# Kernel tuning notes

Hardware: AMD Instinct MI355X
Metric: run time of the kernel (lower is better)

Reference implementation:

```python
import jax, jax.numpy as jnp
from jax import lax
import numpy as np

B, S, D, H = 4, 2048, 1024, 16
HD = D // H
EPS = 1e-8
LN_EPS = 1e-5


def setup_inputs() -> dict:
    key = jax.random.key(0)
    ks = jax.random.split(key, 8)
    sc = 1.0 / np.sqrt(D)  # ~ torch Linear default init scale
    return {
        "x": jax.random.normal(ks[0], (B, S, D), jnp.float32),
        "time_mix_r": jnp.full((1, 1, D), 0.5, jnp.float32),
        "time_mix_k": jnp.full((1, 1, D), 0.5, jnp.float32),
        "time_mix_v": jnp.full((1, 1, D), 0.5, jnp.float32),
        "W_r": jax.random.normal(ks[1], (D, D), jnp.float32) * sc,
        "W_k": jax.random.normal(ks[2], (D, D), jnp.float32) * sc,
        "W_v": jax.random.normal(ks[3], (D, D), jnp.float32) * sc,
        "W_o": jax.random.normal(ks[4], (D, D), jnp.float32) * sc,
        "time_decay": jax.random.normal(ks[5], (H, HD), jnp.float32) * 0.1 - 5.0,
        "time_first": jax.random.normal(ks[6], (H, HD), jnp.float32) * 0.1,
        "ln_gamma": jnp.ones((D,), jnp.float32),
        "ln_beta": jnp.zeros((D,), jnp.float32),
    }


def reference(x, time_mix_r, time_mix_k, time_mix_v, W_r, W_k, W_v, W_o,
              time_decay, time_first, ln_gamma, ln_beta):
    b, s, d = x.shape
    h, hd = time_decay.shape
    # token shift: shifted[t] = x[t-1], zeros at t=0
    shifted = jnp.pad(x[:, :-1, :], ((0, 0), (1, 0), (0, 0)))
    xr = x * time_mix_r + shifted * (1.0 - time_mix_r)
    xk = x * time_mix_k + shifted * (1.0 - time_mix_k)
    xv = x * time_mix_v + shifted * (1.0 - time_mix_v)
    r = (xr @ W_r.T).reshape(b, s, h, hd)
    k = (xk @ W_k.T).reshape(b, s, h, hd)
    v = (xv @ W_v.T).reshape(b, s, h, hd)

    w = -jnp.exp(time_decay)   # (h, hd), negative decay
    u = time_first             # (h, hd)

    def step(carry, kv):
        a, bst = carry          # (b,h,hd) each: numerator state, log-denominator state
        kt, vt = kv             # (b,h,hd)
        wk = kt + u
        p = jnp.maximum(bst, wk)
        e1 = jnp.exp(bst - p)
        e2 = jnp.exp(wk - p)
        out = (e1 * a + e2 * vt) / (e1 + e2 + EPS)
        ww = bst + w
        p2 = jnp.maximum(ww, kt)
        e1b = jnp.exp(ww - p2)
        e2b = jnp.exp(kt - p2)
        a_new = e1b * a + e2b * vt
        b_new = p2 + jnp.log(e1b + e2b + EPS)
        return (a_new, b_new), out

    a0 = jnp.zeros((b, h, hd), x.dtype)
    b0 = jnp.full((b, h, hd), -1e38, x.dtype)
    kT = jnp.moveaxis(k, 1, 0)  # (s,b,h,hd)
    vT = jnp.moveaxis(v, 1, 0)
    _, outs = lax.scan(step, (a0, b0), (kT, vT))
    wkv = jnp.moveaxis(outs, 0, 1)  # (b,s,h,hd)

    rwkv = jax.nn.sigmoid(r) * wkv  # (b,s,h,hd)
    # GroupNorm(num_groups=h, channels=d) applied over (channel-within-group, seq)
    mean = jnp.mean(rwkv, axis=(1, 3), keepdims=True)
    var = jnp.var(rwkv, axis=(1, 3), keepdims=True)
    normed = (rwkv - mean) * lax.rsqrt(var + LN_EPS)
    normed = normed * ln_gamma.reshape(1, 1, h, hd) + ln_beta.reshape(1, 1, h, hd)
    return normed.reshape(b, s, d) @ W_o.T
```

## Files before the change

### kernel.cpp

```cpp
#include <hip/hip_runtime.h>
#include <cstdint>
#include <cstddef>

#define B_  4
#define S_  2048
#define D_  1024
#define H_  16
#define HD_ 64
#define M_  (B_ * S_)

#define CHUNKS_ 64
#define CL_     32

typedef __bf16 bf16_t;
typedef bf16_t bf16x8 __attribute__((ext_vector_type(8)));
typedef float  floatx4 __attribute__((ext_vector_type(4)));

__device__ __forceinline__ void async_copy16(const void* gmem, void* lds) {
  __builtin_amdgcn_global_load_lds(
      (__attribute__((address_space(1))) void*)const_cast<void*>(gmem),
      (__attribute__((address_space(3))) void*)lds,
      16, 0, 0);
}

__global__ void pre_kernel(const float* __restrict__ w0, const float* __restrict__ w1,
                           const float* __restrict__ w2, const float* __restrict__ w3,
                           bf16_t* __restrict__ wout,
                           const float* __restrict__ x,
                           const float* __restrict__ tmr, const float* __restrict__ tmk,
                           const float* __restrict__ tmv,
                           bf16_t* __restrict__ xr, bf16_t* __restrict__ xk,
                           bf16_t* __restrict__ xv) {
  const int ONE_M = 1 << 20;
  int gid = blockIdx.x * blockDim.x + threadIdx.x;
  if (gid < 4 * ONE_M) {
    const float* src = (gid < ONE_M) ? w0 : (gid < 2 * ONE_M) ? w1 : (gid < 3 * ONE_M) ? w2 : w3;
    wout[gid] = (bf16_t)src[gid & (ONE_M - 1)];
  } else {
    int idx = gid - 4 * ONE_M;
    int d = idx & (D_ - 1);
    int t = (idx / D_) & (S_ - 1);
    float xc = x[idx];
    float xp = (t == 0) ? 0.0f : x[idx - D_];
    float mr = tmr[d], mk = tmk[d], mv = tmv[d];
    xr[idx] = (bf16_t)(xc * mr + xp * (1.0f - mr));
    xk[idx] = (bf16_t)(xc * mk + xp * (1.0f - mk));
    xv[idx] = (bf16_t)(xc * mv + xp * (1.0f - mv));
  }
}

#define STG(kt, la, lb, p) do {                                            \
    const char* _ga = Abase + (size_t)(kt) * 128;                          \
    const char* _gb = Bbase + (size_t)(kt) * 128;                          \
    async_copy16(_ga + (size_t)(((p) * 2 + 0) * 64 + r8) * 2048 + cbs,     \
                 (la) + ((p) * 2 + 0) * 8192 + tid * 16);                  \
    async_copy16(_ga + (size_t)(((p) * 2 + 1) * 64 + r8) * 2048 + cbs,     \
                 (la) + ((p) * 2 + 1) * 8192 + tid * 16);                  \
    async_copy16(_gb + (size_t)((p) * 64 + r8) * 2048 + cbs,               \
                 (lb) + (p) * 8192 + tid * 16);                            \
  } while (0)

#define PH1(la, lb, STMT) do {                                             \
    _Pragma("unroll")                                                      \
    for (int _j = 0; _j < 4; ++_j) {                                       \
      const char* _rb = (lb) + (wn * 64 + _j * 16 + l15) * 128;            \
      bfr[_j][0] = *(const bf16x8*)(_rb + ((quad * 16) ^ swz));            \
      bfr[_j][1] = *(const bf16x8*)(_rb + ((64 + quad * 16) ^ swz));       \
    }                                                                      \
    _Pragma("unroll")                                                      \
    for (int _i = 0; _i < 2; ++_i) {                                       \
      const char* _ra = (la) + (wm * 64 + _i * 16 + l15) * 128;            \
      afr[_i][0] = *(const bf16x8*)(_ra + ((quad * 16) ^ swz));            \
      afr[_i][1] = *(const bf16x8*)(_ra + ((64 + quad * 16) ^ swz));       \
    }                                                                      \
    STMT;                                                                  \
    asm volatile("s_waitcnt lgkmcnt(0)" ::: "memory");                     \
    __builtin_amdgcn_sched_barrier(0);                                     \
    __builtin_amdgcn_s_setprio(1);                                         \
    _Pragma("unroll")                                                      \
    for (int _k = 0; _k < 2; ++_k)                                         \
      _Pragma("unroll")                                                    \
      for (int _i = 0; _i < 2; ++_i)                                       \
        _Pragma("unroll")                                                  \
        for (int _j = 0; _j < 4; ++_j)                                     \
          acc[_i][_j] = __builtin_amdgcn_mfma_f32_16x16x32_bf16(           \
              afr[_i][_k], bfr[_j][_k], acc[_i][_j], 0, 0, 0);             \
    __builtin_amdgcn_s_setprio(0);                                         \
  } while (0)

#define PH2(la, STMT) do {                                                 \
    _Pragma("unroll")                                                      \
    for (int _i = 0; _i < 2; ++_i) {                                       \
      const char* _ra = (la) + (wm * 64 + (2 + _i) * 16 + l15) * 128;      \
      afr[_i][0] = *(const bf16x8*)(_ra + ((quad * 16) ^ swz));            \
      afr[_i][1] = *(const bf16x8*)(_ra + ((64 + quad * 16) ^ swz));       \
    }                                                                      \
    STMT;                                                                  \
    asm volatile("s_waitcnt lgkmcnt(0)" ::: "memory");                     \
    __builtin_amdgcn_sched_barrier(0);                                     \
    __builtin_amdgcn_s_setprio(1);                                         \
    _Pragma("unroll")                                                      \
    for (int _k = 0; _k < 2; ++_k)                                         \
      _Pragma("unroll")                                                    \
      for (int _i = 0; _i < 2; ++_i)                                       \
        _Pragma("unroll")                                                  \
        for (int _j = 0; _j < 4; ++_j)                                     \
          acc[2 + _i][_j] = __builtin_amdgcn_mfma_f32_16x16x32_bf16(       \
              afr[_i][_k], bfr[_j][_k], acc[2 + _i][_j], 0, 0, 0);         \
    __builtin_amdgcn_s_setprio(0);                                         \
  } while (0)

#define FENCE_BAR(N) do {                                                  \
    asm volatile("s_waitcnt vmcnt(" #N ")" ::: "memory");                  \
    __builtin_amdgcn_s_barrier();                                          \
    asm volatile("" ::: "memory");                                         \
  } while (0)

template <typename CT>
__device__ __forceinline__ void gemm_core(const bf16_t* __restrict__ A,
                                          const bf16_t* __restrict__ Bw,
                                          CT* __restrict__ C, int m0, int n0) {
  __shared__ __align__(16) bf16_t As[3][256][64];
  __shared__ __align__(16) bf16_t Bs[3][128][64];

  const int tid  = threadIdx.x;
  const int lane = tid & 63;
  const int wave = tid >> 6;
  const int wm   = wave >> 1;
  const int wn   = wave & 1;
  const int l15  = lane & 15;
  const int quad = lane >> 4;
  const int r8   = tid >> 3;
  const int cbs  = (((tid & 7) ^ (r8 & 7)) << 4);
  const int swz  = (l15 & 7) << 4;

  const char* Abase = (const char*)(A + (size_t)m0 * D_);
  const char* Bbase = (const char*)(Bw + (size_t)n0 * D_);

  char* const a0 = (char*)&As[0][0][0];
  char* const a1 = a0 + 32768;
  char* const a2 = a1 + 32768;
  char* const b0 = (char*)&Bs[0][0][0];
  char* const b1 = b0 + 16384;
  char* const b2 = b1 + 16384;

  floatx4 acc[4][4] = {};
  bf16x8 afr[2][2], bfr[4][2];

  STG(0, a0, b0, 0); STG(0, a0, b0, 1);
  STG(1, a1, b1, 0); STG(1, a1, b1, 1);
  FENCE_BAR(6);

  char *aC = a0, *aN = a1, *aF = a2;
  char *bC = b0, *bN = b1, *bF = b2;

#pragma unroll 1
  for (int t = 0; t < 14; ++t) {
    PH1(aC, bC, STG(t + 2, aF, bF, 0));
    PH2(aC,     STG(t + 2, aF, bF, 1));
    FENCE_BAR(6);
    char* x;
    x = aC; aC = aN; aN = aF; aF = x;
    x = bC; bC = bN; bN = bF; bF = x;
  }
  PH1(aC, bC, (void)0);
  PH2(aC,     (void)0);
  FENCE_BAR(0);
  PH1(aN, bN, (void)0);
  PH2(aN,     (void)0);

#pragma unroll
  for (int i = 0; i < 4; ++i) {
#pragma unroll
    for (int j = 0; j < 4; ++j) {
      int row = m0 + wm * 64 + i * 16 + quad * 4;
      int col = n0 + wn * 64 + j * 16 + l15;
      CT* Cp = C + (size_t)row * D_ + col;
#pragma unroll
      for (int r = 0; r < 4; ++r)
        Cp[(size_t)r * D_] = (CT)acc[i][j][r];
    }
  }
}

__global__ __launch_bounds__(512, 2)
void gemm3(const bf16_t* __restrict__ xr, const bf16_t* __restrict__ xk,
           const bf16_t* __restrict__ xv, const bf16_t* __restrict__ Wall,
           bf16_t* __restrict__ rbuf, bf16_t* __restrict__ kbuf, bf16_t* __restrict__ vbuf) {
  const int flat = blockIdx.x;
  const int idx  = (flat & 7) * 96 + (flat >> 3);
  const int proj = idx >> 8;
  const int tt   = idx & 255;
  const int mb   = tt >> 3;
  const int nb   = tt & 7;
  const bf16_t* A  = (proj == 0) ? xr : (proj == 1) ? xk : xv;
  const bf16_t* Bw = Wall + (size_t)proj * (1 << 20);
  bf16_t* C = (proj == 0) ? rbuf : (proj == 1) ? kbuf : vbuf;
  gemm_core<bf16_t>(A, Bw, C, mb * 256, nb * 128);
}

__global__ __launch_bounds__(512, 2)
void gemm_bt(const bf16_t* __restrict__ A, const bf16_t* __restrict__ Bw,
             float* __restrict__ C) {
  const int flat = blockIdx.x;
  const int idx  = (flat & 7) * 32 + (flat >> 3);
  const int mb   = idx >> 3;
  const int nb   = idx & 7;
  gemm_core<float>(A, Bw, C, mb * 256, nb * 128);
}

__device__ __forceinline__ void stage_chunk_bf16(const char* gsrc, char* lds, int lane) {
  const int row = lane >> 3;
  const int cb  = (lane & 7) * 16;
#pragma unroll
  for (int i = 0; i < 4; ++i) {
    size_t go = (size_t)(i * 8 + row) * (D_ * 2) + cb;
    async_copy16(gsrc + go, lds + i * 1024 + lane * 16);
  }
}

__global__ __launch_bounds__(64)
void wkv_pass1(const bf16_t* __restrict__ kbuf, const float* __restrict__ time_decay,
               float* __restrict__ G) {
  __shared__ __align__(16) bf16_t ks[CL_][64];
  const int blk   = blockIdx.x;
  const int chunk = blk & (CHUNKS_ - 1);
  const int bh    = blk >> 6;
  const int b = bh >> 4, h = bh & 15;
  const int lane = threadIdx.x;
  const int c = h * HD_ + lane;
  const float w = -__expf(time_decay[c]);

  const size_t gbase = ((size_t)b * S_ + (size_t)chunk * CL_) * D_ + h * HD_;
  stage_chunk_bf16((const char*)(kbuf + gbase), (char*)&ks[0][0], lane);
  __builtin_amdgcn_s_waitcnt(0);
  __syncthreads();

  float g = -1e38f;
  for (int t = 0; t < CL_; ++t) {
    float kt = (float)ks[t][lane];
    float ww = g + w;
    float d2 = ww - kt;
    float em = __expf(-fabsf(d2));
    float e1b = (d2 >= 0.0f) ? 1.0f : em;
    float e2b = (d2 >= 0.0f) ? em : 1.0f;
    g = fmaxf(ww, kt) + __logf(e1b + e2b + 1e-8f);
  }
  G[(size_t)bh * (CHUNKS_ * 64) + chunk * 64 + lane] = g;
}

__global__ __launch_bounds__(64)
void wkv_pass2(const bf16_t* __restrict__ kbuf, const bf16_t* __restrict__ vbuf,
               const float* __restrict__ time_decay, const float* __restrict__ G,
               float* __restrict__ si_b, float* __restrict__ cs_A, float* __restrict__ cs_Bv) {
  __shared__ __align__(16) float Gs[CHUNKS_][64];
  __shared__ __align__(16) bf16_t ks[CL_][64];
  __shared__ __align__(16) bf16_t vs[CL_][64];
  const int blk   = blockIdx.x;
  const int chunk = blk & (CHUNKS_ - 1);
  const int bh    = blk >> 6;
  const int b = bh >> 4, h = bh & 15;
  const int lane = threadIdx.x;
  const int c = h * HD_ + lane;
  const float w  = -__expf(time_decay[c]);
  const float wL = w * (float)CL_;

  const char* gg = (const char*)(G + (size_t)bh * (CHUNKS_ * 64));
#pragma unroll
  for (int i = 0; i < 16; ++i)
    async_copy16(gg + i * 1024 + lane * 16, (char*)&Gs[0][0] + i * 1024 + lane * 16);

  const size_t gbase = ((size_t)b * S_ + (size_t)chunk * CL_) * D_ + h * HD_;
  stage_chunk_bf16((const char*)(kbuf + gbase), (char*)&ks[0][0], lane);
  stage_chunk_bf16((const char*)(vbuf + gbase), (char*)&vs[0][0], lane);
  __builtin_amdgcn_s_waitcnt(0);
  __syncthreads();

  float bst = -1e38f;
  for (int ch = 0; ch < chunk; ++ch) {
    float g = Gs[ch][lane];
    float b1 = bst + wL;
    float dd = b1 - g;
    float em = __expf(-fabsf(dd));
    bst = fmaxf(b1, g) + __logf(1.0f + em);
  }
  const size_t so = (size_t)bh * (CHUNKS_ * 64) + chunk * 64 + lane;
  si_b[so] = bst;

  float a = 0.0f, Ap = 1.0f;
  for (int t = 0; t < CL_; ++t) {
    float kt = (float)ks[t][lane], vt = (float)vs[t][lane];
    float ww = bst + w;
    float d2 = ww - kt;
    float em = __expf(-fabsf(d2));
    float e1b = (d2 >= 0.0f) ? 1.0f : em;
    float e2b = (d2 >= 0.0f) ? em : 1.0f;
    a  = e1b * a + e2b * vt;
    Ap = Ap * e1b;
    bst = fmaxf(ww, kt) + __logf(e1b + e2b + 1e-8f);
  }
  cs_A [so] = Ap;
  cs_Bv[so] = a;
}

__global__ __launch_bounds__(64)
void wkv_pass3(const bf16_t* __restrict__ rbuf, const bf16_t* __restrict__ kbuf,
               const bf16_t* __restrict__ vbuf,
               const float* __restrict__ time_decay, const float* __restrict__ time_first,
               const float* __restrict__ si_b,
               const float* __restrict__ cs_A, const float* __restrict__ cs_Bv,
               bf16_t* __restrict__ rwkv, float* __restrict__ psum, float* __restrict__ psq) {
  __shared__ __align__(16) char smem[32 * 1024];
  float (*As_)[64] = (float(*)[64])smem;
  float (*Bs_)[64] = (float(*)[64])(smem + 16384);
  const int blk   = blockIdx.x;
  const int chunk = blk & (CHUNKS_ - 1);
  const int bh    = blk >> 6;
  const int b = bh >> 4, h = bh & 15;
  const int lane = threadIdx.x;
  const int c = h * HD_ + lane;
  const float w = -__expf(time_decay[c]);
  const float u = time_first[c];

  const char* ag = (const char*)(cs_A  + (size_t)bh * (CHUNKS_ * 64));
  const char* bg = (const char*)(cs_Bv + (size_t)bh * (CHUNKS_ * 64));
#pragma unroll
  for (int i = 0; i < 16; ++i) {
    async_copy16(ag + i * 1024 + lane * 16, (char*)&As_[0][0] + i * 1024 + lane * 16);
    async_copy16(bg + i * 1024 + lane * 16, (char*)&Bs_[0][0] + i * 1024 + lane * 16);
  }
  const size_t so = (size_t)bh * (CHUNKS_ * 64) + chunk * 64 + lane;
  float bst = si_b[so];
  __builtin_amdgcn_s_waitcnt(0);
  __syncthreads();

  float a = 0.0f;
  for (int ch = 0; ch < chunk; ++ch)
    a = As_[ch][lane] * a + Bs_[ch][lane];
  __syncthreads();

  bf16_t (*rs)[64] = (bf16_t(*)[64])smem;
  bf16_t (*ks)[64] = (bf16_t(*)[64])(smem + 4096);
  bf16_t (*vs)[64] = (bf16_t(*)[64])(smem + 8192);
  const size_t gbase = ((size_t)b * S_ + (size_t)chunk * CL_) * D_ + h * HD_;
  stage_chunk_bf16((const char*)(rbuf + gbase), (char*)&rs[0][0], lane);
  stage_chunk_bf16((const char*)(kbuf + gbase), (char*)&ks[0][0], lane);
  stage_chunk_bf16((const char*)(vbuf + gbase), (char*)&vs[0][0], lane);
  __builtin_amdgcn_s_waitcnt(0);
  __syncthreads();

  float sum = 0.0f, sq = 0.0f;
  size_t widx = gbase + lane;
  for (int t = 0; t < CL_; ++t) {
    float kt = (float)ks[t][lane], vt = (float)vs[t][lane], rt = (float)rs[t][lane];
    float wk = kt + u;
    float d1 = bst - wk;
    float em1 = __expf(-fabsf(d1));
    float e1 = (d1 >= 0.0f) ? 1.0f : em1;
    float e2 = (d1 >= 0.0f) ? em1 : 1.0f;
    float out = __fdividef(e1 * a + e2 * vt, e1 + e2 + 1e-8f);

    float ww = bst + w;
    float d2 = ww - kt;
    float em2 = __expf(-fabsf(d2));
    float e1b = (d2 >= 0.0f) ? 1.0f : em2;
    float e2b = (d2 >= 0.0f) ? em2 : 1.0f;
    a   = e1b * a + e2b * vt;
    bst = fmaxf(ww, kt) + __logf(e1b + e2b + 1e-8f);

    float sig = __fdividef(1.0f, 1.0f + __expf(-rt));
    float o2 = sig * out;
    rwkv[widx] = (bf16_t)o2;
    sum += o2; sq += o2 * o2;
    widx += D_;
  }

#pragma unroll
  for (int off = 32; off > 0; off >>= 1) {
    sum += __shfl_down(sum, off);
    sq  += __shfl_down(sq, off);
  }
  if (lane == 0) {
    psum[bh * CHUNKS_ + chunk] = sum;
    psq [bh * CHUNKS_ + chunk] = sq;
  }
}

__global__ __launch_bounds__(256)
void norm_cast(const bf16_t* __restrict__ rwkv,
               const float* __restrict__ psum, const float* __restrict__ psq,
               const float* __restrict__ gamma, const float* __restrict__ beta,
               bf16_t* __restrict__ normed) {
  __shared__ float smean[4], srstd[4];
  const int tid = threadIdx.x;
  const int lane = tid & 63;
  const int wj = tid >> 6;
  int idx0 = blockIdx.x * 256;
  int d0 = idx0 & (D_ - 1);
  int bb = idx0 / (S_ * D_);
  int bh = bb * H_ + (d0 >> 6) + wj;

  float s = psum[bh * CHUNKS_ + lane];
  float q = psq [bh * CHUNKS_ + lane];
#pragma unroll
  for (int off = 32; off > 0; off >>= 1) {
    s += __shfl_down(s, off);
    q += __shfl_down(q, off);
  }
  if (lane == 0) {
    const float n = (float)(S_ * HD_);
    float mean = s / n;
    float var  = q / n - mean * mean;
    smean[wj] = mean;
    srstd[wj] = rsqrtf(var + 1e-5f);
  }
  __syncthreads();

  int idx = idx0 + tid;
  int d = idx & (D_ - 1);
  float v = ((float)rwkv[idx] - smean[wj]) * srstd[wj] * gamma[d] + beta[d];
  normed[idx] = (bf16_t)v;
}

extern "C" void kernel_launch(void* const* d_in, const int* in_sizes, int n_in,
                              void* d_out, int out_size, void* d_ws, size_t ws_size,
                              hipStream_t stream) {
  const float* x     = (const float*)d_in[0];
  const float* tmr   = (const float*)d_in[1];
  const float* tmk   = (const float*)d_in[2];
  const float* tmv   = (const float*)d_in[3];
  const float* Wr    = (const float*)d_in[4];
  const float* Wk    = (const float*)d_in[5];
  const float* Wv    = (const float*)d_in[6];
  const float* Wo    = (const float*)d_in[7];
  const float* td    = (const float*)d_in[8];
  const float* tf    = (const float*)d_in[9];
  const float* gamma = (const float*)d_in[10];
  const float* beta  = (const float*)d_in[11];

  char* ws = (char*)d_ws;
  const size_t MB = 1024 * 1024;
  bf16_t* W_bf    = (bf16_t*)(ws + 0 * MB);
  bf16_t* Wo_bf   = (bf16_t*)(ws + 6 * MB);
  bf16_t* xr      = (bf16_t*)(ws + 8 * MB);
  bf16_t* xk      = (bf16_t*)(ws + 24 * MB);
  bf16_t* xv      = (bf16_t*)(ws + 40 * MB);
  float*  G       = (float*)(ws + 24 * MB);
  float*  cs_A    = (float*)(ws + 25 * MB);
  float*  cs_Bv   = (float*)(ws + 26 * MB);
  float*  si_b    = (float*)(ws + 27 * MB);
  float*  psum    = (float*)(ws + 28 * MB);
  float*  psq     = (float*)(ws + 28 * MB + 64 * 1024);
  bf16_t* rwkv    = (bf16_t*)(ws + 30 * MB);
  bf16_t* rbuf    = (bf16_t*)(ws + 56 * MB);
  bf16_t* kbuf    = (bf16_t*)(ws + 72 * MB);
  bf16_t* vbuf    = (bf16_t*)(ws + 88 * MB);
  bf16_t* normed  = xr;

  float* outp = (float*)d_out;

  pre_kernel<<<(12 * 1024 * 1024) / 256, 256, 0, stream>>>(
      Wr, Wk, Wv, Wo, W_bf, x, tmr, tmk, tmv, xr, xk, xv);

  gemm3<<<768, 512, 0, stream>>>(xr, xk, xv, W_bf, rbuf, kbuf, vbuf);

  wkv_pass1<<<B_ * H_ * CHUNKS_, 64, 0, stream>>>(kbuf, td, G);
  wkv_pass2<<<B_ * H_ * CHUNKS_, 64, 0, stream>>>(kbuf, vbuf, td, G, si_b, cs_A, cs_Bv);
  wkv_pass3<<<B_ * H_ * CHUNKS_, 64, 0, stream>>>(rbuf, kbuf, vbuf, td, tf,
                                                  si_b, cs_A, cs_Bv, rwkv, psum, psq);

  norm_cast<<<(M_ * D_) / 256, 256, 0, stream>>>(rwkv, psum, psq, gamma, beta, normed);

  gemm_bt<<<256, 512, 0, stream>>>(normed, Wo_bf, outp);
}
```

Baseline: 300.6 us.

## Fuse WKV chunked scan passes and GroupNorm into one per-head kernel; vectorize preprocessing

Replaces the three WKV chunk passes and the separate norm kernel with one kernel per (batch, head). Sixteen wavefronts each handle a 128-step chunk and exchange chunk states and norm partial sums through shared memory, which removes launches and global round-trips for the intermediate state. The preprocessing kernel now converts weights and token-shift mixes four elements per thread with vector loads and stores. The trade-off is only 64 blocks of 1024 threads, so many CUs sit idle. Each thread also runs a longer serial scan, reading k/v/r straight from global memory with strided accesses instead of staging them in LDS.

```diff
diff --git a/kernel.cpp b/kernel.cpp
--- a/kernel.cpp
+++ b/kernel.cpp
@@ -9,11 +9,12 @@
 #define HD_ 64
 #define M_  (B_ * S_)
 
-#define CHUNKS_ 64
-#define CL_     32
+#define WC_ 16
+#define WL_ 128
 
 typedef __bf16 bf16_t;
 typedef bf16_t bf16x8 __attribute__((ext_vector_type(8)));
+typedef bf16_t bf16x4 __attribute__((ext_vector_type(4)));
 typedef float  floatx4 __attribute__((ext_vector_type(4)));
 
 __device__ __forceinline__ void async_copy16(const void* gmem, void* lds) {
@@ -31,21 +32,41 @@
                            const float* __restrict__ tmv,
                            bf16_t* __restrict__ xr, bf16_t* __restrict__ xk,
                            bf16_t* __restrict__ xv) {
-  const int ONE_M = 1 << 20;
+  const int WQ = 1 << 18;
   int gid = blockIdx.x * blockDim.x + threadIdx.x;
-  if (gid < 4 * ONE_M) {
-    const float* src = (gid < ONE_M) ? w0 : (gid < 2 * ONE_M) ? w1 : (gid < 3 * ONE_M) ? w2 : w3;
-    wout[gid] = (bf16_t)src[gid & (ONE_M - 1)];
+  if (gid < 4 * WQ) {
+    int sel = gid >> 18;
+    const float* src = sel == 0 ? w0 : sel == 1 ? w1 : sel == 2 ? w2 : w3;
+    int e = (gid & (WQ - 1)) << 2;
+    const float4 v = *(const float4*)(src + e);
+    bf16x4 o = { (bf16_t)v.x, (bf16_t)v.y, (bf16_t)v.z, (bf16_t)v.w };
+    *(bf16x4*)(wout + ((size_t)gid << 2)) = o;
   } else {
-    int idx = gid - 4 * ONE_M;
-    int d = idx & (D_ - 1);
-    int t = (idx / D_) & (S_ - 1);
-    float xc = x[idx];
-    float xp = (t == 0) ? 0.0f : x[idx - D_];
-    float mr = tmr[d], mk = tmk[d], mv = tmv[d];
-    xr[idx] = (bf16_t)(xc * mr + xp * (1.0f - mr));
-    xk[idx] = (bf16_t)(xc * mk + xp * (1.0f - mk));
-    xv[idx] = (bf16_t)(xc * mv + xp * (1.0f - mv));
+    int g2 = gid - 4 * WQ;
+    size_t idx = (size_t)g2 << 2;
+    int d = (int)(idx & (D_ - 1));
+    int t = (int)((idx >> 10) & (S_ - 1));
+    float4 xc = *(const float4*)(x + idx);
+    float4 xp = make_float4(0.f, 0.f, 0.f, 0.f);
+    if (t != 0) xp = *(const float4*)(x + idx - D_);
+    float4 mr = *(const float4*)(tmr + d);
+    float4 mk = *(const float4*)(tmk + d);
+    float4 mv = *(const float4*)(tmv + d);
+    bf16x4 orv = { (bf16_t)(xc.x * mr.x + xp.x * (1.f - mr.x)),
+                   (bf16_t)(xc.y * mr.y + xp.y * (1.f - mr.y)),
+                   (bf16_t)(xc.z * mr.z + xp.z * (1.f - mr.z)),
+                   (bf16_t)(xc.w * mr.w + xp.w * (1.f - mr.w)) };
+    bf16x4 okv = { (bf16_t)(xc.x * mk.x + xp.x * (1.f - mk.x)),
+                   (bf16_t)(xc.y * mk.y + xp.y * (1.f - mk.y)),
+                   (bf16_t)(xc.z * mk.z + xp.z * (1.f - mk.z)),
+                   (bf16_t)(xc.w * mk.w + xp.w * (1.f - mk.w)) };
+    bf16x4 ovv = { (bf16_t)(xc.x * mv.x + xp.x * (1.f - mv.x)),
+                   (bf16_t)(xc.y * mv.y + xp.y * (1.f - mv.y)),
+                   (bf16_t)(xc.z * mv.z + xp.z * (1.f - mv.z)),
+                   (bf16_t)(xc.w * mv.w + xp.w * (1.f - mv.w)) };
+    *(bf16x4*)(xr + idx) = orv;
+    *(bf16x4*)(xk + idx) = okv;
+    *(bf16x4*)(xv + idx) = ovv;
   }
 }
 
@@ -209,217 +230,143 @@
   gemm_core<float>(A, Bw, C, mb * 256, nb * 128);
 }
 
-__device__ __forceinline__ void stage_chunk_bf16(const char* gsrc, char* lds, int lane) {
-  const int row = lane >> 3;
-  const int cb  = (lane & 7) * 16;
-#pragma unroll
-  for (int i = 0; i < 4; ++i) {
-    size_t go = (size_t)(i * 8 + row) * (D_ * 2) + cb;
-    async_copy16(gsrc + go, lds + i * 1024 + lane * 16);
-  }
-}
-
-__global__ __launch_bounds__(64)
-void wkv_pass1(const bf16_t* __restrict__ kbuf, const float* __restrict__ time_decay,
-               float* __restrict__ G) {
-  __shared__ __align__(16) bf16_t ks[CL_][64];
-  const int blk   = blockIdx.x;
-  const int chunk = blk & (CHUNKS_ - 1);
-  const int bh    = blk >> 6;
+__global__ __launch_bounds__(1024)
+void wkv_gn(const bf16_t* __restrict__ rbuf, const bf16_t* __restrict__ kbuf,
+            const bf16_t* __restrict__ vbuf,
+            const float* __restrict__ time_decay, const float* __restrict__ time_first,
+            const float* __restrict__ gamma, const float* __restrict__ beta,
+            bf16_t* __restrict__ rwkv, bf16_t* __restrict__ normed) {
+  __shared__ float Gs[WC_][64];
+  __shared__ float As_[WC_][64];
+  __shared__ float Bs_[WC_][64];
+  __shared__ float redS[WC_], redQ[WC_];
+  __shared__ float s_stats[2];
+
+  const int bh    = blockIdx.x;
+  const int tid   = threadIdx.x;
+  const int chunk = tid >> 6;
+  const int lane  = tid & 63;
   const int b = bh >> 4, h = bh & 15;
-  const int lane = threadIdx.x;
-  const int c = h * HD_ + lane;
-  const float w = -__expf(time_decay[c]);
-
-  const size_t gbase = ((size_t)b * S_ + (size_t)chunk * CL_) * D_ + h * HD_;
-  stage_chunk_bf16((const char*)(kbuf + gbase), (char*)&ks[0][0], lane);
-  __builtin_amdgcn_s_waitcnt(0);
-  __syncthreads();
-
-  float g = -1e38f;
-  for (int t = 0; t < CL_; ++t) {
-    float kt = (float)ks[t][lane];
-    float ww = g + w;
-    float d2 = ww - kt;
-    float em = __expf(-fabsf(d2));
-    float e1b = (d2 >= 0.0f) ? 1.0f : em;
-    float e2b = (d2 >= 0.0f) ? em : 1.0f;
-    g = fmaxf(ww, kt) + __logf(e1b + e2b + 1e-8f);
-  }
-  G[(size_t)bh * (CHUNKS_ * 64) + chunk * 64 + lane] = g;
-}
-
-__global__ __launch_bounds__(64)
-void wkv_pass2(const bf16_t* __restrict__ kbuf, const bf16_t* __restrict__ vbuf,
-               const float* __restrict__ time_decay, const float* __restrict__ G,
-               float* __restrict__ si_b, float* __restrict__ cs_A, float* __restrict__ cs_Bv) {
-  __shared__ __align__(16) float Gs[CHUNKS_][64];
-  __shared__ __align__(16) bf16_t ks[CL_][64];
-  __shared__ __align__(16) bf16_t vs[CL_][64];
-  const int blk   = blockIdx.x;
-  const int chunk = blk & (CHUNKS_ - 1);
-  const int bh    = blk >> 6;
-  const int b = bh >> 4, h = bh & 15;
-  const int lane = threadIdx.x;
-  const int c = h * HD_ + lane;
-  const float w  = -__expf(time_decay[c]);
-  const float wL = w * (float)CL_;
-
-  const char* gg = (const char*)(G + (size_t)bh * (CHUNKS_ * 64));
-#pragma unroll
-  for (int i = 0; i < 16; ++i)
-    async_copy16(gg + i * 1024 + lane * 16, (char*)&Gs[0][0] + i * 1024 + lane * 16);
-
-  const size_t gbase = ((size_t)b * S_ + (size_t)chunk * CL_) * D_ + h * HD_;
-  stage_chunk_bf16((const char*)(kbuf + gbase), (char*)&ks[0][0], lane);
-  stage_chunk_bf16((const char*)(vbuf + gbase), (char*)&vs[0][0], lane);
-  __builtin_amdgcn_s_waitcnt(0);
-  __syncthreads();
-
-  float bst = -1e38f;
-  for (int ch = 0; ch < chunk; ++ch) {
-    float g = Gs[ch][lane];
-    float b1 = bst + wL;
-    float dd = b1 - g;
-    float em = __expf(-fabsf(dd));
-    bst = fmaxf(b1, g) + __logf(1.0f + em);
-  }
-  const size_t so = (size_t)bh * (CHUNKS_ * 64) + chunk * 64 + lane;
-  si_b[so] = bst;
-
-  float a = 0.0f, Ap = 1.0f;
-  for (int t = 0; t < CL_; ++t) {
-    float kt = (float)ks[t][lane], vt = (float)vs[t][lane];
-    float ww = bst + w;
-    float d2 = ww - kt;
-    float em = __expf(-fabsf(d2));
-    float e1b = (d2 >= 0.0f) ? 1.0f : em;
-    float e2b = (d2 >= 0.0f) ? em : 1.0f;
-    a  = e1b * a + e2b * vt;
-    Ap = Ap * e1b;
-    bst = fmaxf(ww, kt) + __logf(e1b + e2b + 1e-8f);
-  }
-  cs_A [so] = Ap;
-  cs_Bv[so] = a;
-}
-
-__global__ __launch_bounds__(64)
-void wkv_pass3(const bf16_t* __restrict__ rbuf, const bf16_t* __restrict__ kbuf,
-               const bf16_t* __restrict__ vbuf,
-               const float* __restrict__ time_decay, const float* __restrict__ time_first,
-               const float* __restrict__ si_b,
-               const float* __restrict__ cs_A, const float* __restrict__ cs_Bv,
-               bf16_t* __restrict__ rwkv, float* __restrict__ psum, float* __restrict__ psq) {
-  __shared__ __align__(16) char smem[32 * 1024];
-  float (*As_)[64] = (float(*)[64])smem;
-  float (*Bs_)[64] = (float(*)[64])(smem + 16384);
-  const int blk   = blockIdx.x;
-  const int chunk = blk & (CHUNKS_ - 1);
-  const int bh    = blk >> 6;
-  const int b = bh >> 4, h = bh & 15;
-  const int lane = threadIdx.x;
   const int c = h * HD_ + lane;
   const float w = -__expf(time_decay[c]);
   const float u = time_first[c];
 
-  const char* ag = (const char*)(cs_A  + (size_t)bh * (CHUNKS_ * 64));
-  const char* bg = (const char*)(cs_Bv + (size_t)bh * (CHUNKS_ * 64));
+  const size_t gbase = ((size_t)b * S_ + (size_t)chunk * WL_) * D_ + h * HD_ + lane;
+  const bf16_t* kg = kbuf + gbase;
+  const bf16_t* vg = vbuf + gbase;
+  const bf16_t* rg = rbuf + gbase;
+
+  {
+    float g = -1e38f;
+#pragma unroll 4
+    for (int t = 0; t < WL_; ++t) {
+      float kt = (float)kg[(size_t)t * D_];
+      float ww = g + w;
+      float d2 = ww - kt;
+      float em = __expf(-fabsf(d2));
+      float e1b = (d2 >= 0.0f) ? 1.0f : em;
+      float e2b = (d2 >= 0.0f) ? em : 1.0f;
+      g = fmaxf(ww, kt) + __logf(e1b + e2b + 1e-8f);
+    }
+    Gs[chunk][lane] = g;
+  }
+  __syncthreads();
+
+  const float wL = w * (float)WL_;
+  float bst = -1e38f;
+  for (int ch = 0; ch < chunk; ++ch) {
+    float gv = Gs[ch][lane];
+    float b1 = bst + wL;
+    float dd = b1 - gv;
+    float em = __expf(-fabsf(dd));
+    bst = fmaxf(b1, gv) + __logf(1.0f + em);
+  }
+  const float bst_in = bst;
+
+  {
+    float a = 0.0f, Ap = 1.0f;
+#pragma unroll 4
+    for (int t = 0; t < WL_; ++t) {
+      float kt = (float)kg[(size_t)t * D_];
+      float vt = (float)vg[(size_t)t * D_];
+      float ww = bst + w;
+      float d2 = ww - kt;
+      float em = __expf(-fabsf(d2));
+      float e1b = (d2 >= 0.0f) ? 1.0f : em;
+      float e2b = (d2 >= 0.0f) ? em : 1.0f;
+      a  = e1b * a + e2b * vt;
+      Ap = Ap * e1b;
+      bst = fmaxf(ww, kt) + __logf(e1b + e2b + 1e-8f);
+    }
+    As_[chunk][lane] = Ap;
+    Bs_[chunk][lane] = a;
+  }
+  __syncthreads();
+
+  {
+    float a = 0.0f;
+    for (int ch = 0; ch < chunk; ++ch)
+      a = As_[ch][lane] * a + Bs_[ch][lane];
+    bst = bst_in;
+
+    float sum = 0.0f, sq = 0.0f;
+    bf16_t* wg = rwkv + gbase;
+#pragma unroll 4
+    for (int t = 0; t < WL_; ++t) {
+      float kt = (float)kg[(size_t)t * D_];
+      float vt = (float)vg[(size_t)t * D_];
+      float rt = (float)rg[(size_t)t * D_];
+      float wk = kt + u;
+      float d1 = bst - wk;
+      float em1 = __expf(-fabsf(d1));
+      float e1 = (d1 >= 0.0f) ? 1.0f : em1;
+      float e2 = (d1 >= 0.0f) ? em1 : 1.0f;
+      float out = __fdividef(e1 * a + e2 * vt, e1 + e2 + 1e-8f);
+
+      float ww = bst + w;
+      float d2 = ww - kt;
+      float em2 = __expf(-fabsf(d2));
+      float e1b = (d2 >= 0.0f) ? 1.0f : em2;
+      float e2b = (d2 >= 0.0f) ? em2 : 1.0f;
+      a   = e1b * a + e2b * vt;
+      bst = fmaxf(ww, kt) + __logf(e1b + e2b + 1e-8f);
+
+      float sig = __fdividef(1.0f, 1.0f + __expf(-rt));
+      float o = sig * out;
+      wg[(size_t)t * D_] = (bf16_t)o;
+      sum += o; sq += o * o;
+    }
+
 #pragma unroll
-  for (int i = 0; i < 16; ++i) {
-    async_copy16(ag + i * 1024 + lane * 16, (char*)&As_[0][0] + i * 1024 + lane * 16);
-    async_copy16(bg + i * 1024 + lane * 16, (char*)&Bs_[0][0] + i * 1024 + lane * 16);
-  }
-  const size_t so = (size_t)bh * (CHUNKS_ * 64) + chunk * 64 + lane;
-  float bst = si_b[so];
-  __builtin_amdgcn_s_waitcnt(0);
+    for (int off = 32; off > 0; off >>= 1) {
+      sum += __shfl_down(sum, off);
+      sq  += __shfl_down(sq, off);
+    }
+    if (lane == 0) { redS[chunk] = sum; redQ[chunk] = sq; }
+  }
   __syncthreads();
 
-  float a = 0.0f;
-  for (int ch = 0; ch < chunk; ++ch)
-    a = As_[ch][lane] * a + Bs_[ch][lane];
-  __syncthreads();
-
-  bf16_t (*rs)[64] = (bf16_t(*)[64])smem;
-  bf16_t (*ks)[64] = (bf16_t(*)[64])(smem + 4096);
-  bf16_t (*vs)[64] = (bf16_t(*)[64])(smem + 8192);
-  const size_t gbase = ((size_t)b * S_ + (size_t)chunk * CL_) * D_ + h * HD_;
-  stage_chunk_bf16((const char*)(rbuf + gbase), (char*)&rs[0][0], lane);
-  stage_chunk_bf16((const char*)(kbuf + gbase), (char*)&ks[0][0], lane);
-  stage_chunk_bf16((const char*)(vbuf + gbase), (char*)&vs[0][0], lane);
-  __builtin_amdgcn_s_waitcnt(0);
-  __syncthreads();
-
-  float sum = 0.0f, sq = 0.0f;
-  size_t widx = gbase + lane;
-  for (int t = 0; t < CL_; ++t) {
-    float kt = (float)ks[t][lane], vt = (float)vs[t][lane], rt = (float)rs[t][lane];
-    float wk = kt + u;
-    float d1 = bst - wk;
-    float em1 = __expf(-fabsf(d1));
-    float e1 = (d1 >= 0.0f) ? 1.0f : em1;
-    float e2 = (d1 >= 0.0f) ? em1 : 1.0f;
-    float out = __fdividef(e1 * a + e2 * vt, e1 + e2 + 1e-8f);
-
-    float ww = bst + w;
-    float d2 = ww - kt;
-    float em2 = __expf(-fabsf(d2));
-    float e1b = (d2 >= 0.0f) ? 1.0f : em2;
-    float e2b = (d2 >= 0.0f) ? em2 : 1.0f;
-    a   = e1b * a + e2b * vt;
-    bst = fmaxf(ww, kt) + __logf(e1b + e2b + 1e-8f);
-
-    float sig = __fdividef(1.0f, 1.0f + __expf(-rt));
-    float o2 = sig * out;
-    rwkv[widx] = (bf16_t)o2;
-    sum += o2; sq += o2 * o2;
-    widx += D_;
-  }
-
+  if (tid == 0) {
+    float s = 0.0f, q = 0.0f;
 #pragma unroll
-  for (int off = 32; off > 0; off >>= 1) {
-    sum += __shfl_down(sum, off);
-    sq  += __shfl_down(sq, off);
-  }
-  if (lane == 0) {
-    psum[bh * CHUNKS_ + chunk] = sum;
-    psq [bh * CHUNKS_ + chunk] = sq;
-  }
-}
-
-__global__ __launch_bounds__(256)
-void norm_cast(const bf16_t* __restrict__ rwkv,
-               const float* __restrict__ psum, const float* __restrict__ psq,
-               const float* __restrict__ gamma, const float* __restrict__ beta,
-               bf16_t* __restrict__ normed) {
-  __shared__ float smean[4], srstd[4];
-  const int tid = threadIdx.x;
-  const int lane = tid & 63;
-  const int wj = tid >> 6;
-  int idx0 = blockIdx.x * 256;
-  int d0 = idx0 & (D_ - 1);
-  int bb = idx0 / (S_ * D_);
-  int bh = bb * H_ + (d0 >> 6) + wj;
-
-  float s = psum[bh * CHUNKS_ + lane];
-  float q = psq [bh * CHUNKS_ + lane];
-#pragma unroll
-  for (int off = 32; off > 0; off >>= 1) {
-    s += __shfl_down(s, off);
-    q += __shfl_down(q, off);
-  }
-  if (lane == 0) {
+    for (int i = 0; i < WC_; ++i) { s += redS[i]; q += redQ[i]; }
     const float n = (float)(S_ * HD_);
     float mean = s / n;
     float var  = q / n - mean * mean;
-    smean[wj] = mean;
-    srstd[wj] = rsqrtf(var + 1e-5f);
+    s_stats[0] = mean;
+    s_stats[1] = rsqrtf(var + 1e-5f);
   }
   __syncthreads();
-
-  int idx = idx0 + tid;
-  int d = idx & (D_ - 1);
-  float v = ((float)rwkv[idx] - smean[wj]) * srstd[wj] * gamma[d] + beta[d];
-  normed[idx] = (bf16_t)v;
+  {
+    const float mean = s_stats[0];
+    const float gm   = gamma[c] * s_stats[1];
+    const float bt   = beta[c];
+    const bf16_t* wg = rwkv + gbase;
+    bf16_t* og = normed + gbase;
+#pragma unroll 4
+    for (int t = 0; t < WL_; ++t)
+      og[(size_t)t * D_] = (bf16_t)(((float)wg[(size_t)t * D_] - mean) * gm + bt);
+  }
 }
 
 extern "C" void kernel_launch(void* const* d_in, const int* in_sizes, int n_in,
@@ -445,12 +392,6 @@
   bf16_t* xr      = (bf16_t*)(ws + 8 * MB);
   bf16_t* xk      = (bf16_t*)(ws + 24 * MB);
   bf16_t* xv      = (bf16_t*)(ws + 40 * MB);
-  float*  G       = (float*)(ws + 24 * MB);
-  float*  cs_A    = (float*)(ws + 25 * MB);
-  float*  cs_Bv   = (float*)(ws + 26 * MB);
-  float*  si_b    = (float*)(ws + 27 * MB);
-  float*  psum    = (float*)(ws + 28 * MB);
-  float*  psq     = (float*)(ws + 28 * MB + 64 * 1024);
   bf16_t* rwkv    = (bf16_t*)(ws + 30 * MB);
   bf16_t* rbuf    = (bf16_t*)(ws + 56 * MB);
   bf16_t* kbuf    = (bf16_t*)(ws + 72 * MB);
@@ -459,17 +400,13 @@
 
   float* outp = (float*)d_out;
 
-  pre_kernel<<<(12 * 1024 * 1024) / 256, 256, 0, stream>>>(
+  pre_kernel<<<(3 * 1024 * 1024) / 256, 256, 0, stream>>>(
       Wr, Wk, Wv, Wo, W_bf, x, tmr, tmk, tmv, xr, xk, xv);
 
   gemm3<<<768, 512, 0, stream>>>(xr, xk, xv, W_bf, rbuf, kbuf, vbuf);
 
-  wkv_pass1<<<B_ * H_ * CHUNKS_, 64, 0, stream>>>(kbuf, td, G);
-  wkv_pass2<<<B_ * H_ * CHUNKS_, 64, 0, stream>>>(kbuf, vbuf, td, G, si_b, cs_A, cs_Bv);
-  wkv_pass3<<<B_ * H_ * CHUNKS_, 64, 0, stream>>>(rbuf, kbuf, vbuf, td, tf,
-                                                  si_b, cs_A, cs_Bv, rwkv, psum, psq);
-
-  norm_cast<<<(M_ * D_) / 256, 256, 0, stream>>>(rwkv, psum, psq, gamma, beta, normed);
+  wkv_gn<<<B_ * H_, 1024, 0, stream>>>(rbuf, kbuf, vbuf, td, tf,
+                                       gamma, beta, rwkv, normed);
 
   gemm_bt<<<256, 512, 0, stream>>>(normed, Wo_bf, outp);
 }
```

Result: slower. 320.0 us (+6.4%).
